# Kernel tuning notes

Hardware: AMD Instinct MI355X
Metric: run time of the kernel (lower is better)

The kernel has to match this reference:

```python
import jax, jax.numpy as jnp
import numpy as np

CODEBOOK_SIZE = 4096
DIM = 64


def setup_inputs() -> dict:
    key = jax.random.key(0)
    kx, ke = jax.random.split(key)
    x = jax.random.normal(kx, (8, 4096, DIM), dtype=jnp.float32)
    embed = jax.random.normal(ke, (CODEBOOK_SIZE, DIM), dtype=jnp.float32)  # codebook [K, d]
    return {"x": x, "embed": embed}


def reference(x, embed):
    # Eval-mode forward of EuclideanCodebook (svq_temp=None -> argmax).
    shape = x.shape
    flatten = x.reshape(-1, shape[-1])            # [N, d]
    embed_sq = jnp.sum(embed * embed, axis=-1)    # [K]
    # dist = 2 * x @ embed.T - ||embed||^2  (negative squared distance up to a const in x)
    dist = 2.0 * jnp.matmul(flatten, embed.T) - embed_sq[None, :]  # [N, K]
    embed_ind = jnp.argmax(dist, axis=-1)         # [N]
    embed_ind = embed_ind.reshape(shape[:-1])     # [...]
    quantize = embed[embed_ind]                   # gather -> [..., d]
    return (quantize, embed_ind)
```

## Files before the change

### kernel.cpp

```cpp
#include <hip/hip_runtime.h>
#include <math.h>

#define N_ROWS 32768
#define K_CODES 4096
#define DIM 64
#define SPLITS 4
#define TILES_TOTAL (K_CODES / 32)
#define TILES_PER_SPLIT (TILES_TOTAL / SPLITS)
#define PHASES (TILES_PER_SPLIT / 2)
#define QUANT_ELEMS (N_ROWS * DIM)

typedef _Float16 half8 __attribute__((ext_vector_type(8)));
typedef float floatx16 __attribute__((ext_vector_type(16)));

__device__ __forceinline__ void gld16(const void* g, void* l) {
    __builtin_amdgcn_global_load_lds(
        (const __attribute__((address_space(1))) unsigned int*)g,
        (__attribute__((address_space(3))) unsigned int*)l, 16, 0, 0);
}

__global__ void prep_kernel(const float* __restrict__ embed,
                            float* __restrict__ sq, half8* __restrict__ ehi,
                            half8* __restrict__ elo) {
    __shared__ float part[256];
    const int tid = threadIdx.x;
    const int t = blockIdx.x * 256 + tid;
    const int l = t & 63;
    const int s = (t >> 6) & 3;
    const int c = blockIdx.x;
    const int col = l & 31;
    const int code = c * 32 + col;
    const int koff = (l >> 5) * 8 + 16 * s;
    const float* src = embed + (size_t)code * DIM + koff;
    half8 h, lo;
    float ss = 0.f;
#pragma unroll
    for (int j = 0; j < 8; ++j) {
        float v = src[j];
        ss = fmaf(v, v, ss);
        _Float16 hi = (_Float16)v;
        h[j] = hi;
        lo[j] = (_Float16)(v - (float)hi);
    }
    ehi[t] = h;
    elo[t] = lo;
    part[tid] = ss;
    __syncthreads();
    if (tid < 32) {
        float a = 0.f;
#pragma unroll
        for (int q = 0; q < 8; ++q) a += part[tid + 32 * (q & 1) + 64 * (q >> 1)];
        sq[c * 32 + tid] = a;
    }
}

#define SUBTILE(LH, LL, NSQ, CIDX)                                            \
    {                                                                         \
        const half8* lh = (const half8*)(LH);                                 \
        const half8* ll = (const half8*)(LL);                                 \
        floatx16 a0, a1;                                                      \
        _Pragma("unroll") for (int r = 0; r < 16; ++r) {                      \
            a0[r] = (NSQ);                                                    \
            a1[r] = (NSQ);                                                    \
        }                                                                     \
        half8 b;                                                              \
        __builtin_amdgcn_s_setprio(1);                                        \
        b = lh[lane];                                                         \
        a0 = __builtin_amdgcn_mfma_f32_32x32x16_f16(ah[0], b, a0, 0, 0, 0);   \
        a1 = __builtin_amdgcn_mfma_f32_32x32x16_f16(ah[4], b, a1, 0, 0, 0);   \
        a0 = __builtin_amdgcn_mfma_f32_32x32x16_f16(al[0], b, a0, 0, 0, 0);   \
        a1 = __builtin_amdgcn_mfma_f32_32x32x16_f16(al[4], b, a1, 0, 0, 0);   \
        b = lh[64 + lane];                                                    \
        a0 = __builtin_amdgcn_mfma_f32_32x32x16_f16(ah[1], b, a0, 0, 0, 0);   \
        a1 = __builtin_amdgcn_mfma_f32_32x32x16_f16(ah[5], b, a1, 0, 0, 0);   \
        a0 = __builtin_amdgcn_mfma_f32_32x32x16_f16(al[1], b, a0, 0, 0, 0);   \
        a1 = __builtin_amdgcn_mfma_f32_32x32x16_f16(al[5], b, a1, 0, 0, 0);   \
        b = lh[128 + lane];                                                   \
        a0 = __builtin_amdgcn_mfma_f32_32x32x16_f16(ah[2], b, a0, 0, 0, 0);   \
        a1 = __builtin_amdgcn_mfma_f32_32x32x16_f16(ah[6], b, a1, 0, 0, 0);   \
        a0 = __builtin_amdgcn_mfma_f32_32x32x16_f16(al[2], b, a0, 0, 0, 0);   \
        a1 = __builtin_amdgcn_mfma_f32_32x32x16_f16(al[6], b, a1, 0, 0, 0);   \
        b = lh[192 + lane];                                                   \
        a0 = __builtin_amdgcn_mfma_f32_32x32x16_f16(ah[3], b, a0, 0, 0, 0);   \
        a1 = __builtin_amdgcn_mfma_f32_32x32x16_f16(ah[7], b, a1, 0, 0, 0);   \
        a0 = __builtin_amdgcn_mfma_f32_32x32x16_f16(al[3], b, a0, 0, 0, 0);   \
        a1 = __builtin_amdgcn_mfma_f32_32x32x16_f16(al[7], b, a1, 0, 0, 0);   \
        b = ll[lane];                                                         \
        a0 = __builtin_amdgcn_mfma_f32_32x32x16_f16(ah[0], b, a0, 0, 0, 0);   \
        a1 = __builtin_amdgcn_mfma_f32_32x32x16_f16(ah[4], b, a1, 0, 0, 0);   \
        b = ll[64 + lane];                                                    \
        a0 = __builtin_amdgcn_mfma_f32_32x32x16_f16(ah[1], b, a0, 0, 0, 0);   \
        a1 = __builtin_amdgcn_mfma_f32_32x32x16_f16(ah[5], b, a1, 0, 0, 0);   \
        b = ll[128 + lane];                                                   \
        a0 = __builtin_amdgcn_mfma_f32_32x32x16_f16(ah[2], b, a0, 0, 0, 0);   \
        a1 = __builtin_amdgcn_mfma_f32_32x32x16_f16(ah[6], b, a1, 0, 0, 0);   \
        b = ll[192 + lane];                                                   \
        a0 = __builtin_amdgcn_mfma_f32_32x32x16_f16(ah[3], b, a0, 0, 0, 0);   \
        a1 = __builtin_amdgcn_mfma_f32_32x32x16_f16(ah[7], b, a1, 0, 0, 0);   \
        __builtin_amdgcn_s_setprio(0);                                        \
        const int cidx = (CIDX);                                              \
        _Pragma("unroll") for (int r = 0; r < 16; ++r) {                      \
            if (a0[r] > best[r]) {     \
                best[r] = a0[r];                                              \
                bidx[r] = cidx;                                               \
            }                                                                 \
            if (a1[r] > best[16 + r]) {                                       \
                best[16 + r] = a1[r];                                         \
                bidx[16 + r] = cidx;                                          \
            }                                                                 \
        }                                                                     \
    }

__global__ __launch_bounds__(256, 2) void fused_dist_argmax64(
    const float* __restrict__ x, const float* __restrict__ sq,
    const half8* __restrict__ ehi, const half8* __restrict__ elo,
    float* __restrict__ pbest, int* __restrict__ pidx) {
    __shared__ __align__(16) char lbuf[2][16384];
    const int tid = threadIdx.x;
    const int lane = tid & 63;
    const int wave = tid >> 6;
    const int col = lane & 31;
    const int half_ = lane >> 5;
    const int row_base = blockIdx.x * 256 + wave * 64;
    const int split = blockIdx.y;
    const int c0 = split * TILES_PER_SPLIT;

    half8 ah[8], al[8];
#pragma unroll
    for (int g = 0; g < 2; ++g) {
        const float* xs =
            x + (size_t)(row_base + g * 32 + col) * DIM + half_ * 8;
#pragma unroll
        for (int s = 0; s < 4; ++s) {
            half8 h, lo;
#pragma unroll
            for (int j = 0; j < 8; ++j) {
                float v = 2.0f * xs[16 * s + j];
                _Float16 hi = (_Float16)v;
                h[j] = hi;
                lo[j] = (_Float16)(v - (float)hi);
            }
            ah[g * 4 + s] = h;
            al[g * 4 + s] = lo;
        }
    }

    float best[32];
    int bidx[32];
#pragma unroll
    for (int r = 0; r < 32; ++r) {
        best[r] = -INFINITY;
        bidx[r] = 0;
    }

    const char* gh = (const char*)(ehi + (size_t)c0 * 256);
    const char* gl = (const char*)(elo + (size_t)c0 * 256);
    const float* psq = sq + c0 * 32 + col;

    {
        char* d = lbuf[0];
        gld16(gh + (size_t)tid * 16, d + tid * 16);
        gld16(gl + (size_t)tid * 16, d + 4096 + tid * 16);
        gld16(gh + 4096 + (size_t)tid * 16, d + 8192 + tid * 16);
        gld16(gl + 4096 + (size_t)tid * 16, d + 12288 + tid * 16);
    }
    float nsqA = -psq[0];
    float nsqB = -psq[32];
    asm volatile("s_waitcnt vmcnt(0)" ::: "memory");
    __builtin_amdgcn_s_barrier();
    asm volatile("" ::: "memory");

    for (int p = 0; p < PHASES; ++p) {
        char* bufc = lbuf[p & 1];
        if (p + 1 < PHASES) {
            char* bufn = lbuf[(p & 1) ^ 1];
            const size_t go = (size_t)(2 * p + 2) * 4096;
            gld16(gh + go + (size_t)tid * 16, bufn + tid * 16);
            gld16(gl + go + (size_t)tid * 16, bufn + 4096 + tid * 16);
            gld16(gh + go + 4096 + (size_t)tid * 16, bufn + 8192 + tid * 16);
            gld16(gl + go + 4096 + (size_t)tid * 16, bufn + 12288 + tid * 16);
        }
        const float nsq0 = nsqA, nsq1 = nsqB;
        if (p + 1 < PHASES) {
            nsqA = -psq[(2 * p + 2) * 32];
            nsqB = -psq[(2 * p + 3) * 32];
        }

        SUBTILE(bufc, bufc + 4096, nsq0, (c0 + 2 * p) * 32 + col);
        SUBTILE(bufc + 8192, bufc + 12288, nsq1, (c0 + 2 * p + 1) * 32 + col);

        asm volatile("s_waitcnt vmcnt(0)" ::: "memory");
        __builtin_amdgcn_s_barrier();
        asm volatile("" ::: "memory");
    }

#pragma unroll
    for (int r = 0; r < 32; ++r) {
        float bv = best[r];
        int bi = bidx[r];
#pragma unroll
        for (int d = 1; d < 32; d <<= 1) {
            float ov = __shfl_xor(bv, d);
            int oi = __shfl_xor(bi, d);
            if (ov > bv || (ov == bv && oi < bi)) {
                bv = ov;
                bi = oi;
            }
        }
        if (col == 0) {
            const int rr = r & 15;
            const int row = row_base + (r >> 4) * 32 + (rr & 3) + 8 * (rr >> 2) +
                            4 * half_;
            pbest[(size_t)split * N_ROWS + row] = bv;
            pidx[(size_t)split * N_ROWS + row] = bi;
        }
    }
}

__global__ void combine_kernel(const float* __restrict__ pbest,
                               const int* __restrict__ pidx,
                               const float* __restrict__ embed,
                               float* __restrict__ out) {
    const int t = blockIdx.x * blockDim.x + threadIdx.x;
    const int row = t >> 4;
    const int q = t & 15;
    if (row >= N_ROWS) return;

    float best = -INFINITY;
    int bi = 0;
#pragma unroll
    for (int s = 0; s < SPLITS; ++s) {
        float b = pbest[(size_t)s * N_ROWS + row];
        int i = pidx[(size_t)s * N_ROWS + row];
        if (b > best) {
            best = b;
            bi = i;
        }
    }

    const float4* e4 = reinterpret_cast<const float4*>(embed);
    float4 v = e4[(size_t)bi * (DIM / 4) + q];
    reinterpret_cast<float4*>(out)[(size_t)row * (DIM / 4) + q] = v;
    if (q == 0) {
        out[(size_t)QUANT_ELEMS + row] = (float)bi;
    }
}

extern "C" void kernel_launch(void* const* d_in, const int* in_sizes, int n_in,
                              void* d_out, int out_size, void* d_ws,
                              size_t ws_size, hipStream_t stream) {
    const float* x = (const float*)d_in[0];
    const float* embed = (const float*)d_in[1];
    float* out = (float*)d_out;

    char* ws = (char*)d_ws;
    float* sq = (float*)ws;
    half8* ehi = (half8*)(ws + 16384);
    half8* elo = (half8*)(ws + 16384 + 524288);
    float* pbest = (float*)(ws + 16384 + 2 * 524288);
    int* pidx = (int*)(ws + 16384 + 2 * 524288 + SPLITS * N_ROWS * 4);

    prep_kernel<<<TILES_TOTAL, 256, 0, stream>>>(embed, sq, ehi, elo);

    dim3 grid(N_ROWS / 256, SPLITS);
    fused_dist_argmax64<<<grid, 256, 0, stream>>>(x, sq, ehi, elo, pbest,
                                                  pidx);

    const int combine_threads = N_ROWS * (DIM / 4);
    combine_kernel<<<(combine_threads + 255) / 256, 256, 0, stream>>>(
        pbest, pidx, embed, out);
}
```

Before: 124.7 us.

## Double K-splits and merge partial argmax via packed 64-bit atomicMax keys

Raises the codebook split count from 4 to 8 and the launch bounds to 4 blocks per SM, giving more blocks and more waves per CU. Per-split best values and indices are no longer written to separate arrays; each is packed into a monotonic 64-bit key (order-preserving float bits high, inverted index low) and merged with atomicMax into one per-row key. The combine kernel just decodes the key. This trades many global atomics and a larger register-pressure constraint for higher occupancy and a simpler combine; the keys are zeroed in prep_kernel (32768 threads cover N_ROWS).

```diff
diff --git a/kernel.cpp b/kernel.cpp
--- a/kernel.cpp
+++ b/kernel.cpp
@@ -4,7 +4,7 @@
 #define N_ROWS 32768
 #define K_CODES 4096
 #define DIM 64
-#define SPLITS 4
+#define SPLITS 8
 #define TILES_TOTAL (K_CODES / 32)
 #define TILES_PER_SPLIT (TILES_TOTAL / SPLITS)
 #define PHASES (TILES_PER_SPLIT / 2)
@@ -21,10 +21,12 @@
 
 __global__ void prep_kernel(const float* __restrict__ embed,
                             float* __restrict__ sq, half8* __restrict__ ehi,
-                            half8* __restrict__ elo) {
+                            half8* __restrict__ elo,
+                            unsigned long long* __restrict__ keys) {
     __shared__ float part[256];
     const int tid = threadIdx.x;
     const int t = blockIdx.x * 256 + tid;
+    keys[t] = 0ull;
     const int l = t & 63;
     const int s = (t >> 6) & 3;
     const int c = blockIdx.x;
@@ -54,67 +56,67 @@
     }
 }
 
-#define SUBTILE(LH, LL, NSQ, CIDX)                                            \
-    {                                                                         \
-        const half8* lh = (const half8*)(LH);                                 \
-        const half8* ll = (const half8*)(LL);                                 \
-        floatx16 a0, a1;                                                      \
-        _Pragma("unroll") for (int r = 0; r < 16; ++r) {                      \
-            a0[r] = (NSQ);                                                    \
-            a1[r] = (NSQ);                                                    \
-        }                                                                     \
-        half8 b;                                                              \
-        __builtin_amdgcn_s_setprio(1);                                        \
-        b = lh[lane];                                                         \
-        a0 = __builtin_amdgcn_mfma_f32_32x32x16_f16(ah[0], b, a0, 0, 0, 0);   \
-        a1 = __builtin_amdgcn_mfma_f32_32x32x16_f16(ah[4], b, a1, 0, 0, 0);   \
-        a0 = __builtin_amdgcn_mfma_f32_32x32x16_f16(al[0], b, a0, 0, 0, 0);   \
-        a1 = __builtin_amdgcn_mfma_f32_32x32x16_f16(al[4], b, a1, 0, 0, 0);   \
-        b = lh[64 + lane];                                                    \
-        a0 = __builtin_amdgcn_mfma_f32_32x32x16_f16(ah[1], b, a0, 0, 0, 0);   \
-        a1 = __builtin_amdgcn_mfma_f32_32x32x16_f16(ah[5], b, a1, 0, 0, 0);   \
-        a0 = __builtin_amdgcn_mfma_f32_32x32x16_f16(al[1], b, a0, 0, 0, 0);   \
-        a1 = __builtin_amdgcn_mfma_f32_32x32x16_f16(al[5], b, a1, 0, 0, 0);   \
-        b = lh[128 + lane];                                                   \
-        a0 = __builtin_amdgcn_mfma_f32_32x32x16_f16(ah[2], b, a0, 0, 0, 0);   \
-        a1 = __builtin_amdgcn_mfma_f32_32x32x16_f16(ah[6], b, a1, 0, 0, 0);   \
-        a0 = __builtin_amdgcn_mfma_f32_32x32x16_f16(al[2], b, a0, 0, 0, 0);   \
-        a1 = __builtin_amdgcn_mfma_f32_32x32x16_f16(al[6], b, a1, 0, 0, 0);   \
-        b = lh[192 + lane];                                                   \
-        a0 = __builtin_amdgcn_mfma_f32_32x32x16_f16(ah[3], b, a0, 0, 0, 0);   \
-        a1 = __builtin_amdgcn_mfma_f32_32x32x16_f16(ah[7], b, a1, 0, 0, 0);   \
-        a0 = __builtin_amdgcn_mfma_f32_32x32x16_f16(al[3], b, a0, 0, 0, 0);   \
-        a1 = __builtin_amdgcn_mfma_f32_32x32x16_f16(al[7], b, a1, 0, 0, 0);   \
-        b = ll[lane];                                                         \
-        a0 = __builtin_amdgcn_mfma_f32_32x32x16_f16(ah[0], b, a0, 0, 0, 0);   \
-        a1 = __builtin_amdgcn_mfma_f32_32x32x16_f16(ah[4], b, a1, 0, 0, 0);   \
-        b = ll[64 + lane];                                                    \
-        a0 = __builtin_amdgcn_mfma_f32_32x32x16_f16(ah[1], b, a0, 0, 0, 0);   \
-        a1 = __builtin_amdgcn_mfma_f32_32x32x16_f16(ah[5], b, a1, 0, 0, 0);   \
-        b = ll[128 + lane];                                                   \
-        a0 = __builtin_amdgcn_mfma_f32_32x32x16_f16(ah[2], b, a0, 0, 0, 0);   \
-        a1 = __builtin_amdgcn_mfma_f32_32x32x16_f16(ah[6], b, a1, 0, 0, 0);   \
-        b = ll[192 + lane];                                                   \
-        a0 = __builtin_amdgcn_mfma_f32_32x32x16_f16(ah[3], b, a0, 0, 0, 0);   \
-        a1 = __builtin_amdgcn_mfma_f32_32x32x16_f16(ah[7], b, a1, 0, 0, 0);   \
-        __builtin_amdgcn_s_setprio(0);                                        \
-        const int cidx = (CIDX);                                              \
-        _Pragma("unroll") for (int r = 0; r < 16; ++r) {                      \
-            if (a0[r] > best[r]) {     \
-                best[r] = a0[r];                                              \
-                bidx[r] = cidx;                                               \
-            }                                                                 \
-            if (a1[r] > best[16 + r]) {                                       \
-                best[16 + r] = a1[r];                                         \
-                bidx[16 + r] = cidx;                                          \
-            }                                                                 \
-        }                                                                     \
-    }
-
-__global__ __launch_bounds__(256, 2) void fused_dist_argmax64(
+#define SUBTILE(LH, LL, NSQ, CIDX)                                           \
+    {                                                                        \
+        const half8* lh = (const half8*)(LH);                                \
+        const half8* ll = (const half8*)(LL);                                \
+        floatx16 a0, a1;                                                     \
+        _Pragma("unroll") for (int r = 0; r < 16; ++r) {                     \
+            a0[r] = (NSQ);                                                   \
+            a1[r] = (NSQ);                                                   \
+        }                                                                    \
+        half8 b;                                                             \
+        __builtin_amdgcn_s_setprio(1);                                       \
+        b = lh[lane];                                                        \
+        a0 = __builtin_amdgcn_mfma_f32_32x32x16_f16(ah[0], b, a0, 0, 0, 0);  \
+        a1 = __builtin_amdgcn_mfma_f32_32x32x16_f16(ah[4], b, a1, 0, 0, 0);  \
+        a0 = __builtin_amdgcn_mfma_f32_32x32x16_f16(al[0], b, a0, 0, 0, 0);  \
+        a1 = __builtin_amdgcn_mfma_f32_32x32x16_f16(al[4], b, a1, 0, 0, 0);  \
+        b = lh[64 + lane];                                                   \
+        a0 = __builtin_amdgcn_mfma_f32_32x32x16_f16(ah[1], b, a0, 0, 0, 0);  \
+        a1 = __builtin_amdgcn_mfma_f32_32x32x16_f16(ah[5], b, a1, 0, 0, 0);  \
+        a0 = __builtin_amdgcn_mfma_f32_32x32x16_f16(al[1], b, a0, 0, 0, 0);  \
+        a1 = __builtin_amdgcn_mfma_f32_32x32x16_f16(al[5], b, a1, 0, 0, 0);  \
+        b = lh[128 + lane];                                                  \
+        a0 = __builtin_amdgcn_mfma_f32_32x32x16_f16(ah[2], b, a0, 0, 0, 0);  \
+        a1 = __builtin_amdgcn_mfma_f32_32x32x16_f16(ah[6], b, a1, 0, 0, 0);  \
+        a0 = __builtin_amdgcn_mfma_f32_32x32x16_f16(al[2], b, a0, 0, 0, 0);  \
+        a1 = __builtin_amdgcn_mfma_f32_32x32x16_f16(al[6], b, a1, 0, 0, 0);  \
+        b = lh[192 + lane];                                                  \
+        a0 = __builtin_amdgcn_mfma_f32_32x32x16_f16(ah[3], b, a0, 0, 0, 0);  \
+        a1 = __builtin_amdgcn_mfma_f32_32x32x16_f16(ah[7], b, a1, 0, 0, 0);  \
+        a0 = __builtin_amdgcn_mfma_f32_32x32x16_f16(al[3], b, a0, 0, 0, 0);  \
+        a1 = __builtin_amdgcn_mfma_f32_32x32x16_f16(al[7], b, a1, 0, 0, 0);  \
+        b = ll[lane];                                                        \
+        a0 = __builtin_amdgcn_mfma_f32_32x32x16_f16(ah[0], b, a0, 0, 0, 0);  \
+        a1 = __builtin_amdgcn_mfma_f32_32x32x16_f16(ah[4], b, a1, 0, 0, 0);  \
+        b = ll[64 + lane];                                                   \
+        a0 = __builtin_amdgcn_mfma_f32_32x32x16_f16(ah[1], b, a0, 0, 0, 0);  \
+        a1 = __builtin_amdgcn_mfma_f32_32x32x16_f16(ah[5], b, a1, 0, 0, 0);  \
+        b = ll[128 + lane];                                                  \
+        a0 = __builtin_amdgcn_mfma_f32_32x32x16_f16(ah[2], b, a0, 0, 0, 0);  \
+        a1 = __builtin_amdgcn_mfma_f32_32x32x16_f16(ah[6], b, a1, 0, 0, 0);  \
+        b = ll[192 + lane];                                                  \
+        a0 = __builtin_amdgcn_mfma_f32_32x32x16_f16(ah[3], b, a0, 0, 0, 0);  \
+        a1 = __builtin_amdgcn_mfma_f32_32x32x16_f16(ah[7], b, a1, 0, 0, 0);  \
+        __builtin_amdgcn_s_setprio(0);                                       \
+        const int cidx = (CIDX);                                             \
+        _Pragma("unroll") for (int r = 0; r < 16; ++r) {                     \
+            if (a0[r] > best[r]) {    \
+                best[r] = a0[r];                                             \
+                bidx[r] = cidx;                                              \
+            }                                                                \
+            if (a1[r] > best[16 + r]) {                                      \
+                best[16 + r] = a1[r];                                        \
+                bidx[16 + r] = cidx;                                         \
+            }                                                                \
+        }                                                                    \
+    }
+
+__global__ __launch_bounds__(256, 4) void fused_dist_argmax64(
     const float* __restrict__ x, const float* __restrict__ sq,
     const half8* __restrict__ ehi, const half8* __restrict__ elo,
-    float* __restrict__ pbest, int* __restrict__ pidx) {
+    unsigned long long* __restrict__ keys) {
     __shared__ __align__(16) char lbuf[2][16384];
     const int tid = threadIdx.x;
     const int lane = tid & 63;
@@ -209,16 +211,18 @@
         }
         if (col == 0) {
             const int rr = r & 15;
-            const int row = row_base + (r >> 4) * 32 + (rr & 3) + 8 * (rr >> 2) +
-                            4 * half_;
-            pbest[(size_t)split * N_ROWS + row] = bv;
-            pidx[(size_t)split * N_ROWS + row] = bi;
-        }
-    }
-}
-
-__global__ void combine_kernel(const float* __restrict__ pbest,
-                               const int* __restrict__ pidx,
+            const int row = row_base + (r >> 4) * 32 + (rr & 3) +
+                            8 * (rr >> 2) + 4 * half_;
+            unsigned ub = __float_as_uint(bv);
+            unsigned mapped = ub ^ (((int)ub >> 31) | 0x80000000u);
+            unsigned long long key =
+                ((unsigned long long)mapped << 32) | (unsigned)(~bi);
+            atomicMax(keys + row, key);
+        }
+    }
+}
+
+__global__ void combine_kernel(const unsigned long long* __restrict__ keys,
                                const float* __restrict__ embed,
                                float* __restrict__ out) {
     const int t = blockIdx.x * blockDim.x + threadIdx.x;
@@ -226,17 +230,8 @@
     const int q = t & 15;
     if (row >= N_ROWS) return;
 
-    float best = -INFINITY;
-    int bi = 0;
-#pragma unroll
-    for (int s = 0; s < SPLITS; ++s) {
-        float b = pbest[(size_t)s * N_ROWS + row];
-        int i = pidx[(size_t)s * N_ROWS + row];
-        if (b > best) {
-            best = b;
-            bi = i;
-        }
-    }
+    const unsigned long long key = keys[row];
+    const int bi = (int)(~(unsigned)key);
 
     const float4* e4 = reinterpret_cast<const float4*>(embed);
     float4 v = e4[(size_t)bi * (DIM / 4) + q];
@@ -257,16 +252,15 @@
     float* sq = (float*)ws;
     half8* ehi = (half8*)(ws + 16384);
     half8* elo = (half8*)(ws + 16384 + 524288);
-    float* pbest = (float*)(ws + 16384 + 2 * 524288);
-    int* pidx = (int*)(ws + 16384 + 2 * 524288 + SPLITS * N_ROWS * 4);
-
-    prep_kernel<<<TILES_TOTAL, 256, 0, stream>>>(embed, sq, ehi, elo);
+    unsigned long long* keys =
+        (unsigned long long*)(ws + 16384 + 2 * 524288);
+
+    prep_kernel<<<TILES_TOTAL, 256, 0, stream>>>(embed, sq, ehi, elo, keys);
 
     dim3 grid(N_ROWS / 256, SPLITS);
-    fused_dist_argmax64<<<grid, 256, 0, stream>>>(x, sq, ehi, elo, pbest,
-                                                  pidx);
+    fused_dist_argmax64<<<grid, 256, 0, stream>>>(x, sq, ehi, elo, keys);
 
     const int combine_threads = N_ROWS * (DIM / 4);
     combine_kernel<<<(combine_threads + 255) / 256, 256, 0, stream>>>(
-        pbest, pidx, embed, out);
-}
+        keys, embed, out);
+}
```

Measured after the change: 402.4 us. +222.8%, slower.
